# Kernel optimization log

Hardware: AMD Instinct MI355X
Metric: run time of the kernel (lower is better)

The kernel has to match this reference:

```python
import jax, jax.numpy as jnp
import numpy as np

HIDDEN = 2048
NUM_Q_HEADS = 16
NUM_KV_HEADS = 4
HEAD_DIM = HIDDEN // NUM_Q_HEADS  # 128
KV_REP = NUM_Q_HEADS // NUM_KV_HEADS  # 4
KV_DIM = HEAD_DIM * NUM_KV_HEADS


def setup_inputs() -> dict:
    key = jax.random.key(0)
    ks = jax.random.split(key, 9)
    B, S = 2, 2048
    s_in = 1.0 / np.sqrt(HIDDEN)
    return {
        "hidden_states": jax.random.normal(ks[0], (B, S, HIDDEN), dtype=jnp.float32),
        "Wq": jax.random.normal(ks[1], (HIDDEN, HIDDEN), dtype=jnp.float32) * s_in,
        "bq": jnp.zeros((HIDDEN,), dtype=jnp.float32),
        "Wk": jax.random.normal(ks[2], (HIDDEN, KV_DIM), dtype=jnp.float32) * s_in,
        "bk": jnp.zeros((KV_DIM,), dtype=jnp.float32),
        "Wv": jax.random.normal(ks[3], (HIDDEN, KV_DIM), dtype=jnp.float32) * s_in,
        "bv": jnp.zeros((KV_DIM,), dtype=jnp.float32),
        "Wo": jax.random.normal(ks[4], (HIDDEN, HIDDEN), dtype=jnp.float32) * s_in,
        "bo": jnp.zeros((HIDDEN,), dtype=jnp.float32),
    }


def reference(hidden_states, Wq, bq, Wk, bk, Wv, bv, Wo, bo):
    B, S, H = hidden_states.shape
    # projections
    q = hidden_states @ Wq + bq  # [B,S,H]
    k = hidden_states @ Wk + bk  # [B,S,KV_DIM]
    v = hidden_states @ Wv + bv  # [B,S,KV_DIM]
    # [B, heads, S, head_dim]
    q = q.reshape(B, S, NUM_Q_HEADS, HEAD_DIM).transpose(0, 2, 1, 3)
    k = k.reshape(B, S, NUM_KV_HEADS, HEAD_DIM).transpose(0, 2, 1, 3)
    v = v.reshape(B, S, NUM_KV_HEADS, HEAD_DIM).transpose(0, 2, 1, 3)
    # repeat_interleave KV heads to match q heads
    k = jnp.repeat(k, KV_REP, axis=1)  # [B,Hq,S,hd]
    v = jnp.repeat(v, KV_REP, axis=1)
    scale = 1.0 / np.sqrt(HEAD_DIM)
    scores = jnp.einsum('bhqd,bhkd->bhqk', q, k) * scale  # [B,Hq,S,S]
    causal = jnp.triu(jnp.ones((S, S), dtype=bool), k=1)
    scores = jnp.where(causal[None, None], -jnp.inf, scores)
    probs = jax.nn.softmax(scores, axis=-1)
    ctx = jnp.einsum('bhqk,bhkd->bhqd', probs, v)  # [B,Hq,S,hd]
    ctx = ctx.transpose(0, 2, 1, 3).reshape(B, S, H)
    return ctx @ Wo + bo
```

## Files before the change

### kernel.cpp

```cpp
#include <hip/hip_runtime.h>
#include <hip/hip_bf16.h>
#include <stdint.h>

#define SEQ 2048
#define BATCH 2
#define NTOK (SEQ * BATCH)
#define HID 2048
#define NQH 16
#define NKVH 4
#define HD 128
#define KVD 512

typedef __bf16 bf16x8 __attribute__((ext_vector_type(8)));
typedef float f32x4 __attribute__((ext_vector_type(4)));
typedef float f32x16 __attribute__((ext_vector_type(16)));
typedef unsigned int u32;

__device__ __forceinline__ unsigned short f2bf(float f) {
    uint32_t u = __builtin_bit_cast(uint32_t, f);
    uint32_t r = (u + 0x7fffu + ((u >> 16) & 1u)) >> 16;
    return (unsigned short)r;
}

__device__ __forceinline__ u32 cvtpk(float lo, float hi) {
    u32 r;
    asm("v_cvt_pk_bf16_f32 %0, %1, %2" : "=v"(r) : "v"(lo), "v"(hi));
    return r;
}

__device__ __forceinline__ void gload16(const void* g, void* l) {
    __builtin_amdgcn_global_load_lds((const __attribute__((address_space(1))) u32*)g,
                                     (__attribute__((address_space(3))) u32*)l, 16, 0, 0);
}

__global__ void cvt_f32_bf16(const float* __restrict__ in, unsigned short* __restrict__ out, int n4) {
    int i = blockIdx.x * blockDim.x + threadIdx.x;
    int stride = gridDim.x * blockDim.x;
    for (; i < n4; i += stride) {
        float4 v = ((const float4*)in)[i];
        ushort4 o;
        o.x = f2bf(v.x); o.y = f2bf(v.y); o.z = f2bf(v.z); o.w = f2bf(v.w);
        ((ushort4*)out)[i] = o;
    }
}

__global__ __launch_bounds__(256) void transpose_w(const float* __restrict__ W,
                                                   unsigned short* __restrict__ Wt, int N) {
    __shared__ unsigned short tile[64][72];
    const int k0 = blockIdx.x * 64, n0 = blockIdx.y * 64;
    const int t = threadIdx.x;
    const int r = t >> 4;
    const int c4 = (t & 15) * 4;
    #pragma unroll
    for (int i = 0; i < 4; i++) {
        int row = r + i * 16;
        float4 v = *(const float4*)&W[(size_t)(k0 + row) * N + n0 + c4];
        tile[row][c4 + 0] = f2bf(v.x);
        tile[row][c4 + 1] = f2bf(v.y);
        tile[row][c4 + 2] = f2bf(v.z);
        tile[row][c4 + 3] = f2bf(v.w);
    }
    __syncthreads();
    #pragma unroll
    for (int i = 0; i < 4; i++) {
        int nrow = r + i * 16;
        ushort4 o;
        o.x = tile[c4 + 0][nrow];
        o.y = tile[c4 + 1][nrow];
        o.z = tile[c4 + 2][nrow];
        o.w = tile[c4 + 3][nrow];
        *(ushort4*)&Wt[(size_t)(n0 + nrow) * HID + k0 + c4] = o;
    }
}

template <int MODE>
__global__ __launch_bounds__(256) void gemm_tn(const unsigned short* __restrict__ A,
                                               const unsigned short* __restrict__ Bt,
                                               const float* __restrict__ bias,
                                               const float* __restrict__ bias2,
                                               void* __restrict__ out1,
                                               void* __restrict__ out2) {
    __shared__ unsigned short Asm[2][128 * 64];
    __shared__ unsigned short Bsm[2][128 * 64];
    const int m0 = blockIdx.x * 128;
    const int n0 = blockIdx.y * 128;
    const int t = threadIdx.x;
    const int lane = t & 63, w = t >> 6;
    const int wr = (w >> 1) * 64, wc = (w & 1) * 64;
    const int l16 = lane & 15, lg = lane >> 4;

    f32x4 acc[4][4] = {};

    auto stage = [&](int buf, int kt) {
        const int k0 = kt * 64;
        #pragma unroll
        for (int it = 0; it < 4; it++) {
            int base = it * 256 + w * 64;
            int qc = base + lane;
            int row = qc >> 3, c = qc & 7;
            int col = ((c ^ (row & 7)) << 3);
            gload16(&A[(size_t)(m0 + row) * HID + k0 + col], (char*)&Asm[buf][0] + base * 16);
            gload16(&Bt[(size_t)(n0 + row) * HID + k0 + col], (char*)&Bsm[buf][0] + base * 16);
        }
    };

    stage(0, 0);
    __syncthreads();
    int buf = 0;
    for (int kt = 0; kt < HID / 64; kt++) {
        if (kt < HID / 64 - 1) stage(buf ^ 1, kt + 1);
        const char* Ab = (const char*)&Asm[buf][0];
        const char* Bb = (const char*)&Bsm[buf][0];
        #pragma unroll
        for (int kk = 0; kk < 2; kk++) {
            bf16x8 af[4], bfr[4];
            #pragma unroll
            for (int m = 0; m < 4; m++) {
                int row = wr + m * 16 + l16;
                af[m] = *(const bf16x8*)(Ab + row * 128 + (((kk * 4 + lg) ^ (row & 7)) << 4));
            }
            #pragma unroll
            for (int n = 0; n < 4; n++) {
                int row = wc + n * 16 + l16;
                bfr[n] = *(const bf16x8*)(Bb + row * 128 + (((kk * 4 + lg) ^ (row & 7)) << 4));
            }
            #pragma unroll
            for (int m = 0; m < 4; m++)
                #pragma unroll
                for (int n = 0; n < 4; n++)
                    acc[m][n] = __builtin_amdgcn_mfma_f32_16x16x32_bf16(af[m], bfr[n], acc[m][n], 0, 0, 0);
        }
        __syncthreads();
        buf ^= 1;
    }
    #pragma unroll
    for (int m = 0; m < 4; m++) {
        int row = m0 + wr + m * 16 + lg * 4;
        #pragma unroll
        for (int n = 0; n < 4; n++) {
            int col = n0 + wc + n * 16 + l16;
            #pragma unroll
            for (int r = 0; r < 4; r++) {
                float v = acc[m][n][r];
                int rr = row + r;
                if constexpr (MODE == 0) {
                    v = (v + bias[col]) * 0.08838834764831845f;
                    ((unsigned short*)out1)[(size_t)rr * HID + col] = f2bf(v);
                } else if constexpr (MODE == 1) {
                    if (col < 512) {
                        v += bias[col];
                        ((unsigned short*)out1)[(size_t)rr * KVD + col] = f2bf(v);
                    } else {
                        int c2 = col - 512;
                        v += bias2[c2];
                        int b = rr >> 11, s = rr & (SEQ - 1);
                        ((unsigned short*)out2)[((size_t)b * KVD + c2) * SEQ + s] = f2bf(v);
                    }
                } else {
                    v += bias[col];
                    ((float*)out1)[(size_t)rr * HID + col] = v;
                }
            }
        }
    }
}

__global__ __launch_bounds__(256, 2) void attn(const unsigned short* __restrict__ Q,
                                               const unsigned short* __restrict__ K,
                                               const unsigned short* __restrict__ Vt,
                                               unsigned short* __restrict__ ctx) {
    __shared__ unsigned short Ksm[2][64 * 128];
    __shared__ unsigned short Vsm[2][128 * 64];
    const int n = blockIdx.x;
    const int qx = n & 15;
    const int qt = (n < 256) ? (15 - qx) : qx;
    const int bh = (n >> 4) & 31;
    const int b = bh >> 4, h = bh & 15, hk = h >> 2;
    const int t = threadIdx.x, w = t >> 6, lane = t & 63;
    const int lam = lane & 31, hi = lane >> 5;
    const int qw = qt * 128 + w * 32;
    const int qg = qw + lam;
    const size_t qrowbase = (size_t)b * SEQ + qw;

    const unsigned short* Kg = K + (size_t)b * SEQ * KVD + hk * HD;
    const unsigned short* Vg = Vt + ((size_t)b * KVD + hk * HD) * SEQ;

    bf16x8 qf[8];
    #pragma unroll
    for (int kc = 0; kc < 8; kc++)
        qf[kc] = *(const bf16x8*)&Q[(qrowbase + lam) * HID + h * HD + kc * 16 + hi * 8];

    f32x16 oacc[4] = {};
    float m = -1e30f, l = 0.f;

    auto stage = [&](int buf, int kt) {
        const int kvb = kt * 64;
        #pragma unroll
        for (int it = 0; it < 4; it++) {
            int base = it * 256 + w * 64;
            int qc = base + lane;
            {
                int row = qc >> 4, c = qc & 15;
                gload16(&Kg[(size_t)(kvb + row) * KVD + ((c ^ (row & 7)) << 3)],
                        (char*)&Ksm[buf][0] + base * 16);
            }
            {
                int row = qc >> 3, c = qc & 7;
                gload16(&Vg[(size_t)row * SEQ + kvb + ((c ^ (row & 7)) << 3)],
                        (char*)&Vsm[buf][0] + base * 16);
            }
        }
    };

    const int ntile = 2 * qt + 2;
    stage(0, 0);
    __syncthreads();
    int buf = 0;
    for (int kt = 0; kt < ntile; kt++) {
        const int kvb = kt * 64;
        if (kt + 1 < ntile) stage(buf ^ 1, kt + 1);
        if (kvb <= qw + 31) {
            const char* Kb = (const char*)&Ksm[buf][0];
            const char* Vb = (const char*)&Vsm[buf][0];
            f32x16 st0 = {}, st1 = {};
            #pragma unroll
            for (int kc = 0; kc < 8; kc++) {
                int coff = (kc * 32 + hi * 16) ^ ((lam & 7) << 4);
                bf16x8 kf0 = *(const bf16x8*)(Kb + lam * 256 + coff);
                bf16x8 kf1 = *(const bf16x8*)(Kb + (32 + lam) * 256 + coff);
                st0 = __builtin_amdgcn_mfma_f32_32x32x16_bf16(kf0, qf[kc], st0, 0, 0, 0);
                st1 = __builtin_amdgcn_mfma_f32_32x32x16_bf16(kf1, qf[kc], st1, 0, 0, 0);
            }
            if (kvb + 63 > qw) {
                #pragma unroll
                for (int r = 0; r < 16; r++) {
                    int krow = (r & 3) + 8 * (r >> 2) + 4 * hi;
                    if (kvb + krow > qg) st0[r] = -1e30f;
                    if (kvb + 32 + krow > qg) st1[r] = -1e30f;
                }
            }
            float tmax = st0[0];
            #pragma unroll
            for (int r = 1; r < 16; r++) tmax = fmaxf(tmax, st0[r]);
            #pragma unroll
            for (int r = 0; r < 16; r++) tmax = fmaxf(tmax, st1[r]);
            tmax = fmaxf(tmax, __shfl_xor(tmax, 32));
            float mn = fmaxf(m, tmax);
            float sf = __expf(m - mn);
            m = mn;
            float rs = 0.f;
            #pragma unroll
            for (int r = 0; r < 16; r++) { st0[r] = __expf(st0[r] - mn); rs += st0[r]; }
            #pragma unroll
            for (int r = 0; r < 16; r++) { st1[r] = __expf(st1[r] - mn); rs += st1[r]; }
            rs += __shfl_xor(rs, 32);
            l = l * sf + rs;
            #pragma unroll
            for (int dc = 0; dc < 4; dc++)
                #pragma unroll
                for (int r = 0; r < 16; r++) oacc[dc][r] *= sf;
            u32 pw0[4][2], pw1[4][2];
            #pragma unroll
            for (int g = 0; g < 4; g++) {
                pw0[g][0] = cvtpk(st0[4 * g], st0[4 * g + 1]);
                pw0[g][1] = cvtpk(st0[4 * g + 2], st0[4 * g + 3]);
                pw1[g][0] = cvtpk(st1[4 * g], st1[4 * g + 1]);
                pw1[g][1] = cvtpk(st1[4 * g + 2], st1[4 * g + 3]);
            }
            #pragma unroll
            for (int kc = 0; kc < 4; kc++) {
                const u32 (*pw)[2] = (kc >> 1) ? pw1 : pw0;
                int g0 = (kc & 1) * 2;
                u32 own0 = hi ? pw[g0 + 1][0] : pw[g0][0];
                u32 own1 = hi ? pw[g0 + 1][1] : pw[g0][1];
                u32 off0 = hi ? pw[g0][0] : pw[g0 + 1][0];
                u32 off1 = hi ? pw[g0][1] : pw[g0 + 1][1];
                u32 xw0 = __shfl_xor(off0, 32);
                u32 xw1 = __shfl_xor(off1, 32);
                int4 paw;
                paw.x = hi ? xw0 : own0;
                paw.y = hi ? xw1 : own1;
                paw.z = hi ? own0 : xw0;
                paw.w = hi ? own1 : xw1;
                bf16x8 pa = __builtin_bit_cast(bf16x8, paw);
                #pragma unroll
                for (int dc = 0; dc < 4; dc++) {
                    bf16x8 vf = *(const bf16x8*)(Vb + (dc * 32 + lam) * 128 +
                                                 ((kc * 32 + hi * 16) ^ ((lam & 7) << 4)));
                    oacc[dc] = __builtin_amdgcn_mfma_f32_32x32x16_bf16(vf, pa, oacc[dc], 0, 0, 0);
                }
            }
        }
        __syncthreads();
        buf ^= 1;
    }

    float inv = 1.f / l;
    char* osm = (char*)&Ksm[0][0] + w * 8192;
    #pragma unroll
    for (int dc = 0; dc < 4; dc++)
        #pragma unroll
        for (int r = 0; r < 16; r += 2) {
            int d = dc * 32 + (r & 3) + 8 * (r >> 2) + 4 * hi;
            u32 wd = cvtpk(oacc[dc][r] * inv, oacc[dc][r + 1] * inv);
            *(u32*)(osm + lam * 256 + ((d * 2) ^ ((lam & 7) << 4))) = wd;
        }
    __syncthreads();
    const int q2 = lane >> 1, half = lane & 1;
    #pragma unroll
    for (int cc = 0; cc < 8; cc++) {
        bf16x8 v = *(const bf16x8*)(osm + q2 * 256 + (((half * 8 + cc) * 16) ^ ((q2 & 7) << 4)));
        *(bf16x8*)&ctx[(qrowbase + q2) * HID + h * HD + half * 64 + cc * 8] = v;
    }
}

extern "C" void kernel_launch(void* const* d_in, const int* in_sizes, int n_in,
                              void* d_out, int out_size, void* d_ws, size_t ws_size,
                              hipStream_t stream) {
    const float* X  = (const float*)d_in[0];
    const float* Wq = (const float*)d_in[1];
    const float* bq = (const float*)d_in[2];
    const float* Wk = (const float*)d_in[3];
    const float* bk = (const float*)d_in[4];
    const float* Wv = (const float*)d_in[5];
    const float* bv = (const float*)d_in[6];
    const float* Wo = (const float*)d_in[7];
    const float* bo = (const float*)d_in[8];
    float* out = (float*)d_out;

    const size_t MB = 1u << 20;
    char* ws = (char*)d_ws;
    if (ws_size < 76 * MB) return;
    unsigned short* Xb   = (unsigned short*)(ws + 0 * MB);
    unsigned short* Wqt  = (unsigned short*)(ws + 16 * MB);
    unsigned short* Wkvt = (unsigned short*)(ws + 24 * MB);
    unsigned short* Wot  = (unsigned short*)(ws + 28 * MB);
    unsigned short* Qb   = (unsigned short*)(ws + 36 * MB);
    unsigned short* Kb   = (unsigned short*)(ws + 52 * MB);
    unsigned short* Vtb  = (unsigned short*)(ws + 56 * MB);
    unsigned short* Ctx  = (unsigned short*)(ws + 60 * MB);

    cvt_f32_bf16<<<2048, 256, 0, stream>>>(X, Xb, NTOK * HID / 4);
    transpose_w<<<dim3(HID / 64, HID / 64), 256, 0, stream>>>(Wq, Wqt, HID);
    transpose_w<<<dim3(HID / 64, KVD / 64), 256, 0, stream>>>(Wk, Wkvt, KVD);
    transpose_w<<<dim3(HID / 64, KVD / 64), 256, 0, stream>>>(Wv, Wkvt + (size_t)512 * HID, KVD);
    transpose_w<<<dim3(HID / 64, HID / 64), 256, 0, stream>>>(Wo, Wot, HID);

    gemm_tn<0><<<dim3(NTOK / 128, HID / 128), 256, 0, stream>>>(Xb, Wqt, bq, nullptr, Qb, nullptr);
    gemm_tn<1><<<dim3(NTOK / 128, 1024 / 128), 256, 0, stream>>>(Xb, Wkvt, bk, bv, Kb, Vtb);

    attn<<<dim3(512), 256, 0, stream>>>(Qb, Kb, Vtb, Ctx);

    gemm_tn<3><<<dim3(NTOK / 128, HID / 128), 256, 0, stream>>>(Ctx, Wot, bo, nullptr, out, nullptr);
}
```

Measured before the change: 230.5 us.

## Fuse QKV projections into one GEMM and merge weight transposes into one launch

The four weight-transpose launches become a single kernel that picks the source matrix from blockIdx.y. The Q and KV projection GEMMs are merged into one 32x24-block GEMM over a concatenated Wqkv^T, with the epilogue routing columns to Q, K or transposed V. The attention block ordering also changes to interleave all heads per query tile, heaviest tiles first. The goal is fewer launches and a larger single GEMM grid for better CU fill, in exchange for a branchier epilogue and a different L2 reuse pattern in attention.

Result: no change. 227.4 us (-1.3%).

```diff
diff --git a/kernel.cpp b/kernel.cpp
--- a/kernel.cpp
+++ b/kernel.cpp
@@ -44,10 +44,22 @@
     }
 }
 
-__global__ __launch_bounds__(256) void transpose_w(const float* __restrict__ W,
-                                                   unsigned short* __restrict__ Wt, int N) {
+__global__ __launch_bounds__(256) void transpose_all(const float* __restrict__ Wq,
+                                                     const float* __restrict__ Wk,
+                                                     const float* __restrict__ Wv,
+                                                     const float* __restrict__ Wo,
+                                                     unsigned short* __restrict__ Wqkvt,
+                                                     unsigned short* __restrict__ Wot) {
     __shared__ unsigned short tile[64][72];
-    const int k0 = blockIdx.x * 64, n0 = blockIdx.y * 64;
+    const int y = blockIdx.y;
+    const float* W;
+    unsigned short* dst;
+    int N, ny;
+    if (y < 32)      { W = Wq; dst = Wqkvt;                        N = 2048; ny = y; }
+    else if (y < 40) { W = Wk; dst = Wqkvt + (size_t)2048 * HID;   N = 512;  ny = y - 32; }
+    else if (y < 48) { W = Wv; dst = Wqkvt + (size_t)2560 * HID;   N = 512;  ny = y - 40; }
+    else             { W = Wo; dst = Wot;                          N = 2048; ny = y - 48; }
+    const int k0 = blockIdx.x * 64, n0 = ny * 64;
     const int t = threadIdx.x;
     const int r = t >> 4;
     const int c4 = (t & 15) * 4;
@@ -69,17 +81,19 @@
         o.y = tile[c4 + 1][nrow];
         o.z = tile[c4 + 2][nrow];
         o.w = tile[c4 + 3][nrow];
-        *(ushort4*)&Wt[(size_t)(n0 + nrow) * HID + k0 + c4] = o;
+        *(ushort4*)&dst[(size_t)(n0 + nrow) * HID + k0 + c4] = o;
     }
 }
 
 template <int MODE>
-__global__ __launch_bounds__(256) void gemm_tn(const unsigned short* __restrict__ A,
+__global__ __launch_bounds__(256) void gemm128(const unsigned short* __restrict__ A,
                                                const unsigned short* __restrict__ Bt,
-                                               const float* __restrict__ bias,
-                                               const float* __restrict__ bias2,
-                                               void* __restrict__ out1,
-                                               void* __restrict__ out2) {
+                                               const float* __restrict__ b0,
+                                               const float* __restrict__ b1,
+                                               const float* __restrict__ b2,
+                                               void* __restrict__ o0,
+                                               void* __restrict__ o1,
+                                               void* __restrict__ o2) {
     __shared__ unsigned short Asm[2][128 * 64];
     __shared__ unsigned short Bsm[2][128 * 64];
     const int m0 = blockIdx.x * 128;
@@ -133,6 +147,7 @@
         __syncthreads();
         buf ^= 1;
     }
+    const float sc = 0.08838834764831845f;
     #pragma unroll
     for (int m = 0; m < 4; m++) {
         int row = m0 + wr + m * 16 + lg * 4;
@@ -144,21 +159,22 @@
                 float v = acc[m][n][r];
                 int rr = row + r;
                 if constexpr (MODE == 0) {
-                    v = (v + bias[col]) * 0.08838834764831845f;
-                    ((unsigned short*)out1)[(size_t)rr * HID + col] = f2bf(v);
-                } else if constexpr (MODE == 1) {
-                    if (col < 512) {
-                        v += bias[col];
-                        ((unsigned short*)out1)[(size_t)rr * KVD + col] = f2bf(v);
+                    if (col < 2048) {
+                        v = (v + b0[col]) * sc;
+                        ((unsigned short*)o0)[(size_t)rr * HID + col] = f2bf(v);
+                    } else if (col < 2560) {
+                        int c = col - 2048;
+                        v += b1[c];
+                        ((unsigned short*)o1)[(size_t)rr * KVD + c] = f2bf(v);
                     } else {
-                        int c2 = col - 512;
-                        v += bias2[c2];
+                        int c = col - 2560;
+                        v += b2[c];
                         int b = rr >> 11, s = rr & (SEQ - 1);
-                        ((unsigned short*)out2)[((size_t)b * KVD + c2) * SEQ + s] = f2bf(v);
+                        ((unsigned short*)o2)[((size_t)b * KVD + c) * SEQ + s] = f2bf(v);
                     }
                 } else {
-                    v += bias[col];
-                    ((float*)out1)[(size_t)rr * HID + col] = v;
+                    v += b0[col];
+                    ((float*)o0)[(size_t)rr * HID + col] = v;
                 }
             }
         }
@@ -172,9 +188,8 @@
     __shared__ unsigned short Ksm[2][64 * 128];
     __shared__ unsigned short Vsm[2][128 * 64];
     const int n = blockIdx.x;
-    const int qx = n & 15;
-    const int qt = (n < 256) ? (15 - qx) : qx;
-    const int bh = (n >> 4) & 31;
+    const int qt = 15 - (n >> 5);
+    const int bh = n & 31;
     const int b = bh >> 4, h = bh & 15, hk = h >> 2;
     const int t = threadIdx.x, w = t >> 6, lane = t & 63;
     const int lam = lane & 31, hi = lane >> 5;
@@ -331,25 +346,20 @@
     const size_t MB = 1u << 20;
     char* ws = (char*)d_ws;
     if (ws_size < 76 * MB) return;
-    unsigned short* Xb   = (unsigned short*)(ws + 0 * MB);
-    unsigned short* Wqt  = (unsigned short*)(ws + 16 * MB);
-    unsigned short* Wkvt = (unsigned short*)(ws + 24 * MB);
-    unsigned short* Wot  = (unsigned short*)(ws + 28 * MB);
-    unsigned short* Qb   = (unsigned short*)(ws + 36 * MB);
-    unsigned short* Kb   = (unsigned short*)(ws + 52 * MB);
-    unsigned short* Vtb  = (unsigned short*)(ws + 56 * MB);
-    unsigned short* Ctx  = (unsigned short*)(ws + 60 * MB);
+    unsigned short* Xb    = (unsigned short*)(ws + 0 * MB);
+    unsigned short* Wqkvt = (unsigned short*)(ws + 16 * MB);
+    unsigned short* Wot   = (unsigned short*)(ws + 28 * MB);
+    unsigned short* Qb    = (unsigned short*)(ws + 36 * MB);
+    unsigned short* Kb    = (unsigned short*)(ws + 52 * MB);
+    unsigned short* Vtb   = (unsigned short*)(ws + 56 * MB);
+    unsigned short* Ctx   = (unsigned short*)(ws + 60 * MB);
 
     cvt_f32_bf16<<<2048, 256, 0, stream>>>(X, Xb, NTOK * HID / 4);
-    transpose_w<<<dim3(HID / 64, HID / 64), 256, 0, stream>>>(Wq, Wqt, HID);
-    transpose_w<<<dim3(HID / 64, KVD / 64), 256, 0, stream>>>(Wk, Wkvt, KVD);
-    transpose_w<<<dim3(HID / 64, KVD / 64), 256, 0, stream>>>(Wv, Wkvt + (size_t)512 * HID, KVD);
-    transpose_w<<<dim3(HID / 64, HID / 64), 256, 0, stream>>>(Wo, Wot, HID);
-
-    gemm_tn<0><<<dim3(NTOK / 128, HID / 128), 256, 0, stream>>>(Xb, Wqt, bq, nullptr, Qb, nullptr);
-    gemm_tn<1><<<dim3(NTOK / 128, 1024 / 128), 256, 0, stream>>>(Xb, Wkvt, bk, bv, Kb, Vtb);
+    transpose_all<<<dim3(32, 80), 256, 0, stream>>>(Wq, Wk, Wv, Wo, Wqkvt, Wot);
+
+    gemm128<0><<<dim3(32, 24), 256, 0, stream>>>(Xb, Wqkvt, bq, bk, bv, Qb, Kb, Vtb);
 
     attn<<<dim3(512), 256, 0, stream>>>(Qb, Kb, Vtb, Ctx);
 
-    gemm_tn<3><<<dim3(NTOK / 128, HID / 128), 256, 0, stream>>>(Ctx, Wot, bo, nullptr, out, nullptr);
-}
+    gemm128<1><<<dim3(32, 16), 256, 0, stream>>>(Ctx, Wot, bo, nullptr, nullptr, (void*)out, nullptr, nullptr);
+}
```
